# Optimization experiments

Hardware: AMD Instinct MI355X
Metric: run time of the kernel (lower is better)

Reference implementation:

```python
import jax, jax.numpy as jnp
import numpy as np

B, T, N, C = 32, 16, 1000, 16   # batch, seq_len, num_nodes, in_channels
G, H, O = 32, 512, 8            # gcn_hidden, lstm_hidden, output_dim
E_RAND = 8000                   # random edges; + N self loops -> E = 9000


def setup_inputs() -> dict:
    key = jax.random.key(0)
    ks = jax.random.split(key, 13)
    rng = np.random.default_rng(0)
    src = rng.integers(0, N, E_RAND)
    dst = rng.integers(0, N, E_RAND)
    loop = np.arange(N)
    edge_index = jnp.asarray(
        np.stack([np.concatenate([src, loop]), np.concatenate([dst, loop])]),
        dtype=jnp.int32)
    ew = np.concatenate([rng.uniform(0.5, 1.5, E_RAND), np.ones(N)]).astype(np.float32)

    def p(k, s, sc):
        return jax.random.normal(k, s, jnp.float32) * sc

    return {
        'x': p(ks[0], (B, T, N, C), 1.0),
        'edge_index': edge_index,
        'edge_weight': jnp.asarray(ew),
        'gcn_w': p(ks[1], (T, C, G), 0.1),
        'gcn_b': p(ks[2], (T, G), 0.02),
        'w_ih0': p(ks[3], (4 * H, N * G), 0.02),
        'w_hh0': p(ks[4], (4 * H, H), 0.02),
        'b_ih0': p(ks[5], (4 * H,), 0.02),
        'b_hh0': p(ks[6], (4 * H,), 0.02),
        'w_ih1': p(ks[7], (4 * H, H), 0.02),
        'w_hh1': p(ks[8], (4 * H, H), 0.02),
        'b_ih1': p(ks[9], (4 * H,), 0.02),
        'b_hh1': p(ks[10], (4 * H,), 0.02),
        'proj_w': p(ks[11], (O, H), 0.04),
        'proj_b': p(ks[12], (O,), 0.02),
    }


def _lstm_layer(inp, w_ih, w_hh, b_ih, b_hh):
    # inp: [B, T, D]; torch gate order i, f, g, o
    pre = jnp.einsum('btd,gd->btg', inp, w_ih) + b_ih + b_hh  # [B, T, 4H]
    h0 = jnp.zeros((inp.shape[0], w_hh.shape[1]), inp.dtype)

    def step(carry, x_t):
        h, c = carry
        gates = x_t + h @ w_hh.T
        i, f, g, o = jnp.split(gates, 4, axis=-1)
        c = jax.nn.sigmoid(f) * c + jax.nn.sigmoid(i) * jnp.tanh(g)
        h = jax.nn.sigmoid(o) * jnp.tanh(c)
        return (h, c), h

    _, hs = jax.lax.scan(step, (h0, h0), pre.transpose(1, 0, 2))  # [T, B, H]
    return hs.transpose(1, 0, 2)


def reference(x, edge_index, edge_weight, gcn_w, gcn_b,
              w_ih0, w_hh0, b_ih0, b_hh0,
              w_ih1, w_hh1, b_ih1, b_hh1, proj_w, proj_b):
    src, dst = edge_index[0], edge_index[1]
    # GCN symmetric normalization (self-loops already present in edge list)
    deg = jax.ops.segment_sum(edge_weight, dst, num_segments=N)
    dinv = jnp.where(deg > 0, jax.lax.rsqrt(jnp.maximum(deg, 1e-12)), 0.0)
    norm = dinv[src] * edge_weight * dinv[dst]  # [E]
    # per-timestep linear transform: distinct GCN weight per t
    xw = jnp.einsum('btni,tio->btno', x, gcn_w)  # [B, T, N, G]
    # gather from source nodes, scale, scatter-add into targets
    msg = xw[:, :, src, :] * norm[None, None, :, None]      # [B, T, E, G]
    agg = jnp.zeros_like(xw).at[:, :, dst, :].add(msg)      # [B, T, N, G]
    h = jax.nn.relu(agg + gcn_b[None, :, None, :])
    seq = h.reshape(B, T, N * G)                            # [B, T, N*G]
    out1 = _lstm_layer(seq, w_ih0, w_hh0, b_ih0, b_hh0)
    out2 = _lstm_layer(out1, w_ih1, w_hh1, b_ih1, b_hh1)
    last = out2[:, -1, :]                                   # [B, H]
    return last @ proj_w.T + proj_b                         # [B, O]
```

## Files before the change

### kernel.cpp

```cpp
#include <hip/hip_runtime.h>
#include <hip/hip_bf16.h>

typedef unsigned short u16;
typedef __bf16 bf16x8 __attribute__((ext_vector_type(8)));
typedef float f32x4 __attribute__((ext_vector_type(4)));
typedef unsigned short u16x8 __attribute__((ext_vector_type(8)));
typedef unsigned long long u64;

#define NB 32
#define NT 16
#define NN 1000
#define NC 16
#define NG 32
#define NH 512
#define NK 32000
#define BH (NB*NH)
#define LWG 64
#define LTH 384
#define NSPLIT 8

__device__ __forceinline__ u16 f2bf(float f) {
    unsigned int u = __float_as_uint(f);
    unsigned int r = u + 0x7FFFu + ((u >> 16) & 1u);
    return (u16)(r >> 16);
}

__device__ __forceinline__ unsigned cvt2(float a, float b) {
    unsigned r;
    asm("v_cvt_pk_bf16_f32 %0, %1, %2" : "=v"(r) : "v"(a), "v"(b));
    return r;
}

__device__ __forceinline__ float sigmoidf(float x) { return 1.f / (1.f + __expf(-x)); }

__device__ __forceinline__ float dot4(float4 a, float4 b) {
    return a.x * b.x + a.y * b.y + a.z * b.z + a.w * b.w;
}

#define AT_LOAD(p)    __hip_atomic_load((p), __ATOMIC_RELAXED, __HIP_MEMORY_SCOPE_AGENT)
#define AT_STORE(p,v) __hip_atomic_store((p), (v), __ATOMIC_RELAXED, __HIP_MEMORY_SCOPE_AGENT)

#define GLOAD16(g, l) __builtin_amdgcn_global_load_lds( \
    (const __attribute__((address_space(1))) void*)(g),  \
    (__attribute__((address_space(3))) void*)(l), 16, 0, 0)

__global__ void graph_prep(const int* __restrict__ ei, const float* __restrict__ ew, int E,
                           int* __restrict__ rowptr, int* __restrict__ csr_src,
                           float* __restrict__ csr_nrm) {
    __shared__ float degs[NN];
    __shared__ float dinv[NN];
    __shared__ int cnt[NN];
    __shared__ int rp[NN + 1];
    __shared__ int wsum[16];
    int tid = threadIdx.x, lane = tid & 63, wid = tid >> 6;
    for (int n = tid; n < NN; n += 1024) { degs[n] = 0.f; cnt[n] = 0; }
    __syncthreads();
    for (int e = tid; e < E; e += 1024) {
        int d = ei[E + e];
        atomicAdd(&degs[d], ew[e]);
        atomicAdd(&cnt[d], 1);
    }
    __syncthreads();
    for (int n = tid; n < NN; n += 1024) {
        float d = degs[n];
        dinv[n] = d > 0.f ? rsqrtf(fmaxf(d, 1e-12f)) : 0.f;
    }
    int v = (tid < NN) ? cnt[tid] : 0;
    int inc = v;
#pragma unroll
    for (int d = 1; d < 64; d <<= 1) {
        int u = __shfl_up(inc, d, 64);
        if (lane >= d) inc += u;
    }
    if (lane == 63) wsum[wid] = inc;
    __syncthreads();
    if (tid == 0) {
        int a = 0;
#pragma unroll
        for (int i = 0; i < 16; ++i) { int t = wsum[i]; wsum[i] = a; a += t; }
    }
    __syncthreads();
    int excl = inc - v + wsum[wid];
    if (tid <= NN) { rp[tid] = excl; rowptr[tid] = excl; }
    if (tid < NN) cnt[tid] = 0;
    __syncthreads();
    for (int e = tid; e < E; e += 1024) {
        int d = ei[E + e], s = ei[e];
        int pos = rp[d] + atomicAdd(&cnt[d], 1);
        csr_src[pos] = s;
        csr_nrm[pos] = dinv[s] * ew[e] * dinv[d];
    }
}

__global__ __launch_bounds__(1024) void gcn_fused(const float* __restrict__ x,
                                                  const float* __restrict__ gw,
                                                  const float* __restrict__ gb,
                                                  const int* __restrict__ rowptr,
                                                  const int* __restrict__ csr_src,
                                                  const float* __restrict__ csr_nrm,
                                                  u16* __restrict__ seq) {
    __shared__ float xwlds[NN * NG];
    __shared__ float wlds[NC * NG];
    __shared__ int rplds[NN + 1];
    int bt = blockIdx.x;
    int t = bt & 15;
    int tid = threadIdx.x;
    int g = tid & 31, grp = tid >> 5;

    for (int i = tid; i < NC * NG; i += 1024) wlds[i] = gw[t * NC * NG + i];
    for (int i = tid; i <= NN; i += 1024) rplds[i] = rowptr[i];
    __syncthreads();

    const float* xbt = x + (size_t)bt * NN * NC;
    for (int r = grp; r < NN; r += 32) {
        const float4* xr = (const float4*)(xbt + r * NC);
        float4 a0 = xr[0], a1 = xr[1], a2 = xr[2], a3 = xr[3];
        float acc = a0.x * wlds[g]        + a0.y * wlds[32 + g]
                  + a0.z * wlds[64 + g]   + a0.w * wlds[96 + g]
                  + a1.x * wlds[128 + g]  + a1.y * wlds[160 + g]
                  + a1.z * wlds[192 + g]  + a1.w * wlds[224 + g]
                  + a2.x * wlds[256 + g]  + a2.y * wlds[288 + g]
                  + a2.z * wlds[320 + g]  + a2.w * wlds[352 + g]
                  + a3.x * wlds[384 + g]  + a3.y * wlds[416 + g]
                  + a3.z * wlds[448 + g]  + a3.w * wlds[480 + g];
        xwlds[r * NG + g] = acc;
    }
    __syncthreads();

    float bias = gb[t * NG + g];
    u16* seqbt = seq + (size_t)bt * NK;
    for (int n = grp; n < NN; n += 32) {
        int p0 = rplds[n], p1 = rplds[n + 1];
        float acc = 0.f;
        for (int p = p0; p < p1; ++p)
            acc += csr_nrm[p] * xwlds[csr_src[p] * NG + g];
        seqbt[n * NG + g] = f2bf(fmaxf(acc + bias, 0.f));
    }
}

__global__ __launch_bounds__(256) void gemm_f32b(const u16* __restrict__ A,
                                                 const float* __restrict__ Bw,
                                                 float* __restrict__ part) {
    __shared__ __align__(16) u16 As[2][128 * 64];
    __shared__ __align__(16) u16 Bs[2][128 * 64];
    int tid = threadIdx.x;
    int lane = tid & 63, wid = tid >> 6;
    int wr = wid >> 1, wc = wid & 1;
    int bid = blockIdx.x;
    int s = bid & 7;
    int idx = bid >> 3;
    int tm = (idx & 3) * 128, tn = (idx >> 2) * 128;
    int ks0 = s * 62 + (s < 4 ? s : 4);
    int ksn = (s < 4) ? 63 : 62;

    int srow = tid >> 3, sc = tid & 7;
    int sce = sc ^ (srow & 7);
    const u16* gaBase = A + (size_t)(tm + srow) * NK + (size_t)ks0 * 64 + sce * 8;
    int br = tid >> 3, bc = tid & 7;
    int bce = bc ^ (br & 7);
    const float* gbBase = Bw + (size_t)(tn + br) * NK + (size_t)ks0 * 64 + bce * 8;

    f32x4 acc[4][4];
#pragma unroll
    for (int i = 0; i < 4; ++i)
#pragma unroll
        for (int j = 0; j < 4; ++j) acc[i][j] = (f32x4){0.f, 0.f, 0.f, 0.f};

    int fr = lane & 15, kq = lane >> 4, fs = fr & 7;

    float4 bq0[4], bq1[4];
#pragma unroll
    for (int q = 0; q < 4; ++q)
        GLOAD16(gaBase + (size_t)q * 32 * NK, &As[0][0] + srow * 64 + sc * 8 + q * 32 * 64);
#pragma unroll
    for (int q = 0; q < 4; ++q) {
        bq0[q] = *(const float4*)(gbBase + (size_t)q * 32 * NK);
        bq1[q] = *(const float4*)(gbBase + (size_t)q * 32 * NK + 4);
    }
#pragma unroll
    for (int q = 0; q < 4; ++q) {
        uint4 w;
        w.x = cvt2(bq0[q].x, bq0[q].y); w.y = cvt2(bq0[q].z, bq0[q].w);
        w.z = cvt2(bq1[q].x, bq1[q].y); w.w = cvt2(bq1[q].z, bq1[q].w);
        *(uint4*)(&Bs[0][0] + (br + q * 32) * 64 + bc * 8) = w;
    }
    __syncthreads();

    int p = 0;
    for (int ks = 0; ks < ksn; ++ks) {
        bool more = (ks + 1) < ksn;
        if (more) {
            const u16* ga = gaBase + (size_t)(ks + 1) * 64;
#pragma unroll
            for (int q = 0; q < 4; ++q)
                GLOAD16(ga + (size_t)q * 32 * NK, &As[p ^ 1][0] + srow * 64 + sc * 8 + q * 32 * 64);
            const float* gbf = gbBase + (size_t)(ks + 1) * 64;
#pragma unroll
            for (int q = 0; q < 4; ++q) {
                bq0[q] = *(const float4*)(gbf + (size_t)q * 32 * NK);
                bq1[q] = *(const float4*)(gbf + (size_t)q * 32 * NK + 4);
            }
        }
        {
            const u16* Ap = &As[p][0];
            const u16* Bp = &Bs[p][0];
#pragma unroll
            for (int kk = 0; kk < 2; ++kk) {
                int c0 = ((kq + kk * 4) ^ fs) * 8;
                bf16x8 af[4], bv[4];
#pragma unroll
                for (int fm = 0; fm < 4; ++fm)
                    af[fm] = *(const bf16x8*)(Ap + (wr * 64 + fm * 16 + fr) * 64 + c0);
#pragma unroll
                for (int fn = 0; fn < 4; ++fn)
                    bv[fn] = *(const bf16x8*)(Bp + (wc * 64 + fn * 16 + fr) * 64 + c0);
#pragma unroll
                for (int fm = 0; fm < 4; ++fm)
#pragma unroll
                    for (int fn = 0; fn < 4; ++fn)
                        acc[fm][fn] = __builtin_amdgcn_mfma_f32_16x16x32_bf16(af[fm], bv[fn], acc[fm][fn], 0, 0, 0);
            }
        }
        if (more) {
#pragma unroll
            for (int q = 0; q < 4; ++q) {
                uint4 w;
                w.x = cvt2(bq0[q].x, bq0[q].y); w.y = cvt2(bq0[q].z, bq0[q].w);
                w.z = cvt2(bq1[q].x, bq1[q].y); w.w = cvt2(bq1[q].z, bq1[q].w);
                *(uint4*)(&Bs[p ^ 1][0] + (br + q * 32) * 64 + bc * 8) = w;
            }
        }
        __syncthreads();
        p ^= 1;
    }

    int rq = lane >> 4;
    size_t base = (size_t)s * 512 * 2048;
#pragma unroll
    for (int fm = 0; fm < 4; ++fm)
#pragma unroll
        for (int fn = 0; fn < 4; ++fn)
#pragma unroll
            for (int rr = 0; rr < 4; ++rr) {
                int m = tm + wr * 64 + fm * 16 + rq * 4 + rr;
                int n = tn + wc * 64 + fn * 16 + (lane & 15);
                part[base + (size_t)m * 2048 + n] = acc[fm][fn][rr];
            }
}

__global__ __launch_bounds__(256) void reduce_bias_p(const float* __restrict__ part,
                                                     const float* __restrict__ b_ih0,
                                                     const float* __restrict__ b_hh0,
                                                     float* __restrict__ pre0p) {
    int s = blockIdx.y;
    int r = blockIdx.x * 64 + (threadIdx.x & 63);
    int bq = threadIdx.x >> 6;
    float bias = b_ih0[r] + b_hh0[r];
#pragma unroll
    for (int b8 = 0; b8 < 8; ++b8) {
        int b = bq * 8 + b8;
        float acc = bias;
#pragma unroll
        for (int sk = 0; sk < NSPLIT; ++sk)
            acc += part[(size_t)sk * 1048576 + (size_t)(b * 16 + s) * 2048 + r];
        pre0p[((size_t)s * 2048 + r) * 32 + b] = acc;
    }
}

__global__ __launch_bounds__(256) void wperm(const float* __restrict__ w_hh0,
                                             const float* __restrict__ w_ih1,
                                             const float* __restrict__ w_hh1,
                                             u16* __restrict__ Wbig) {
    int rt = blockIdx.x;
    int wg = blockIdx.y;
    int tid = threadIdx.x;
#pragma unroll
    for (int it = 0; it < 4; ++it) {
        int idx = it * 256 + tid;
        int kt = idx >> 6, lane = idx & 63;
        int p = rt * 16 + (lane & 15);
        int gate = (p & 31) >> 3;
        int col = wg * 8 + (p & 7);
        const float* src;
        if (p < 32)      src = w_hh0 + (size_t)(gate * NH + col) * NH;
        else if (p < 64) src = w_ih1 + (size_t)(gate * NH + col) * NH;
        else             src = w_hh1 + (size_t)(gate * NH + col) * NH;
        int k0 = kt * 32 + (lane >> 4) * 8;
        float4 v0 = *(const float4*)(src + k0);
        float4 v1 = *(const float4*)(src + k0 + 4);
        u16x8 o;
        o[0] = f2bf(v0.x); o[1] = f2bf(v0.y); o[2] = f2bf(v0.z); o[3] = f2bf(v0.w);
        o[4] = f2bf(v1.x); o[5] = f2bf(v1.y); o[6] = f2bf(v1.z); o[7] = f2bf(v1.w);
        *(u16x8*)(Wbig + (((size_t)wg * 6 + rt) * 16 + kt) * 512 + lane * 8) = o;
    }
}

__global__ void init2(u16* h0, u16* h1, int* flags) {
    int i = blockIdx.x * 256 + threadIdx.x;
    if (i < 2 * BH) { h0[i] = 0; h1[i] = 0; }
    if (i < 1024) flags[i] = 0;
}

__global__ __launch_bounds__(LTH) void lstm2(const u16* __restrict__ Wbig,
                                             const float* __restrict__ pre0p,
                                             const float* __restrict__ b_ih1,
                                             const float* __restrict__ b_hh1,
                                             u16* __restrict__ h0buf,
                                             u16* __restrict__ h1buf,
                                             float* __restrict__ h1f,
                                             int* __restrict__ flags) {
    __shared__ __align__(16) u16 hA0[32 * 520];
    __shared__ __align__(16) u16 hA1[32 * 520];
    __shared__ float G[96][33];
    __shared__ float cst[2][8][32];
    __shared__ u16 hst[2][8][32];
    int wg = blockIdx.x, tid = threadIdx.x;
    int wid = tid >> 6, lane = tid & 63;
    int grp = wid >> 1;

    bf16x8 af[16];
    const u16* wsrc = Wbig + (size_t)wg * 49152 + wid * 8192 + lane * 8;
#pragma unroll
    for (int kt = 0; kt < 16; ++kt) af[kt] = *(const bf16x8*)(wsrc + kt * 512);

    if (tid < 512) ((float*)cst)[tid] = 0.f;

    int uj = (tid >> 5) & 7, ub = tid & 31;
    int ucol = wg * 8 + uj;
    float bs0 = 0.f, bs1 = 0.f, bs2 = 0.f, bs3 = 0.f;
    if (tid < 256) {
        bs0 = b_ih1[ucol] + b_hh1[ucol];
        bs1 = b_ih1[NH + ucol] + b_hh1[NH + ucol];
        bs2 = b_ih1[2 * NH + ucol] + b_hh1[2 * NH + ucol];
        bs3 = b_ih1[3 * NH + ucol] + b_hh1[3 * NH + ucol];
    }
    __syncthreads();

    for (int s = 0; s <= 16; ++s) {
        for (int r = wid; r < 64; r += 6) {
            const u64* src = (r < 32)
                ? (const u64*)(h0buf + ((s & 1) ^ 1) * BH + r * 512)
                : (const u64*)(h1buf + (s & 1) * BH + (r - 32) * 512);
            u16* dst = (r < 32) ? (hA0 + r * 520) : (hA1 + (r - 32) * 520);
            u64 v0 = AT_LOAD(src + lane);
            u64 v1 = AT_LOAD(src + 64 + lane);
            *(u64*)(dst + lane * 4) = v0;
            *(u64*)(dst + 256 + lane * 4) = v1;
        }
        float up0 = 0.f, up1 = 0.f, up2 = 0.f, up3 = 0.f;
        if (tid < 256 && s < 16) {
            const float* pp = pre0p + (size_t)s * 2048 * 32 + ub;
            up0 = pp[(size_t)ucol * 32];
            up1 = pp[((size_t)NH + ucol) * 32];
            up2 = pp[((size_t)2 * NH + ucol) * 32];
            up3 = pp[((size_t)3 * NH + ucol) * 32];
        }
        __syncthreads();

        bool active = (grp == 0) ? (s < 16) : (s >= 1);
        if (active) {
            const u16* hA = (grp < 2) ? hA0 : hA1;
            const u16* hp = hA + (lane & 15) * 520 + (lane >> 4) * 8;
            f32x4 a0 = (f32x4){0.f, 0.f, 0.f, 0.f};
            f32x4 a1 = (f32x4){0.f, 0.f, 0.f, 0.f};
#pragma unroll
            for (int kt = 0; kt < 16; ++kt) {
                bf16x8 b0 = *(const bf16x8*)(hp + kt * 32);
                bf16x8 b1 = *(const bf16x8*)(hp + 16 * 520 + kt * 32);
                a0 = __builtin_amdgcn_mfma_f32_16x16x32_bf16(af[kt], b0, a0, 0, 0, 0);
                a1 = __builtin_amdgcn_mfma_f32_16x16x32_bf16(af[kt], b1, a1, 0, 0, 0);
            }
            int r0 = wid * 16 + (lane >> 4) * 4;
#pragma unroll
            for (int rr = 0; rr < 4; ++rr) {
                G[r0 + rr][lane & 15] = a0[rr];
                G[r0 + rr][16 + (lane & 15)] = a1[rr];
            }
        }
        __syncthreads();

        if (tid < 256) {
            if (s < 16) {
                float gi = G[uj][ub] + up0;
                float gf = G[8 + uj][ub] + up1;
                float gg = G[16 + uj][ub] + up2;
                float go = G[24 + uj][ub] + up3;
                float c = sigmoidf(gf) * cst[0][uj][ub] + sigmoidf(gi) * tanhf(gg);
                cst[0][uj][ub] = c;
                hst[0][uj][ub] = f2bf(sigmoidf(go) * tanhf(c));
            }
            if (s >= 1) {
                float gi = G[32 + uj][ub] + G[64 + uj][ub] + bs0;
                float gf = G[40 + uj][ub] + G[72 + uj][ub] + bs1;
                float gg = G[48 + uj][ub] + G[80 + uj][ub] + bs2;
                float go = G[56 + uj][ub] + G[88 + uj][ub] + bs3;
                float c = sigmoidf(gf) * cst[1][uj][ub] + sigmoidf(gi) * tanhf(gg);
                cst[1][uj][ub] = c;
                float hv = sigmoidf(go) * tanhf(c);
                hst[1][uj][ub] = f2bf(hv);
                if (s == 16) h1f[ub * NH + ucol] = hv;
            }
        }
        __syncthreads();

        if (s < 16) {
            if (wid == 0) {
                if (lane < 32) {
                    union { u16 a[8]; u64 q[2]; } v;
#pragma unroll
                    for (int j = 0; j < 8; ++j) v.a[j] = hst[0][j][lane];
                    u64* d = (u64*)(h0buf + (s & 1) * BH + lane * 512 + wg * 8);
                    AT_STORE(d, v.q[0]); AT_STORE(d + 1, v.q[1]);
                } else if (s >= 1) {
                    int b = lane - 32;
                    union { u16 a[8]; u64 q[2]; } v;
#pragma unroll
                    for (int j = 0; j < 8; ++j) v.a[j] = hst[1][j][b];
                    u64* d = (u64*)(h1buf + ((s - 1) & 1) * BH + b * 512 + wg * 8);
                    AT_STORE(d, v.q[0]); AT_STORE(d + 1, v.q[1]);
                }
                asm volatile("s_waitcnt vmcnt(0)" ::: "memory");
                if (lane == 0) AT_STORE(&flags[wg * 16], s + 1);
                int target = s + 1;
                for (;;) {
                    int v = AT_LOAD(&flags[lane * 16]);
                    if (__all(v >= target)) break;
                    __builtin_amdgcn_s_sleep(1);
                }
            }
            __syncthreads();
        }
    }
}

__global__ __launch_bounds__(1024) void proj_k(const float* __restrict__ h1f,
                                               const float* __restrict__ proj_w,
                                               const float* __restrict__ proj_b,
                                               float* __restrict__ out) {
    __shared__ float pj[32][8][4];
    int tid = threadIdx.x;
    int b = tid >> 5, o = (tid >> 2) & 7, kq = tid & 3;
    const float4* hp = (const float4*)(h1f + (size_t)b * NH + kq * 128);
    const float4* wp = (const float4*)(proj_w + (size_t)o * NH + kq * 128);
    float acc = 0.f;
#pragma unroll 8
    for (int k = 0; k < 32; ++k) acc += dot4(hp[k], wp[k]);
    pj[b][o][kq] = acc;
    __syncthreads();
    if (tid < 256) {
        int bb = tid >> 3, oo = tid & 7;
        out[bb * 8 + oo] = pj[bb][oo][0] + pj[bb][oo][1] + pj[bb][oo][2] + pj[bb][oo][3] + proj_b[oo];
    }
}

extern "C" void kernel_launch(void* const* d_in, const int* in_sizes, int n_in,
                              void* d_out, int out_size, void* d_ws, size_t ws_size,
                              hipStream_t stream) {
    const float* x      = (const float*)d_in[0];
    const int*   ei     = (const int*)d_in[1];
    const float* ew     = (const float*)d_in[2];
    const float* gcn_w  = (const float*)d_in[3];
    const float* gcn_b  = (const float*)d_in[4];
    const float* w_ih0  = (const float*)d_in[5];
    const float* w_hh0  = (const float*)d_in[6];
    const float* b_ih0  = (const float*)d_in[7];
    const float* b_hh0  = (const float*)d_in[8];
    const float* w_ih1  = (const float*)d_in[9];
    const float* w_hh1  = (const float*)d_in[10];
    const float* b_ih1  = (const float*)d_in[11];
    const float* b_hh1  = (const float*)d_in[12];
    const float* proj_w = (const float*)d_in[13];
    const float* proj_b = (const float*)d_in[14];
    int E = in_sizes[2];

    char* ws = (char*)d_ws;
    size_t off = 0;
    float* part   = (float*)(ws + off);
    u16* Wbig     = (u16*)part;        off += 50331648;
    u16* seq      = (u16*)(ws + off);  off += 32768000;
    float* pre0p  = (float*)(ws + off); off += 4194304;
    u16* h0buf    = (u16*)(ws + off);  off += 2 * BH * 2;
    u16* h1buf    = (u16*)(ws + off);  off += 2 * BH * 2;
    float* h1f    = (float*)(ws + off); off += BH * 4;
    int* flags    = (int*)(ws + off);  off += 4096;
    int* rowptr   = (int*)(ws + off);  off += 4096;
    int* csr_src  = (int*)(ws + off);  off += 36864;
    float* csr_nrm = (float*)(ws + off); off += 36864;
    (void)ws_size; (void)n_in; (void)out_size;

    graph_prep<<<1, 1024, 0, stream>>>(ei, ew, E, rowptr, csr_src, csr_nrm);
    gcn_fused<<<512, 1024, 0, stream>>>(x, gcn_w, gcn_b, rowptr, csr_src, csr_nrm, seq);
    gemm_f32b<<<512, 256, 0, stream>>>(seq, w_ih0, part);
    reduce_bias_p<<<dim3(32, 16), 256, 0, stream>>>(part, b_ih0, b_hh0, pre0p);
    wperm<<<dim3(6, 64), 256, 0, stream>>>(w_hh0, w_ih1, w_hh1, Wbig);
    init2<<<128, 256, 0, stream>>>(h0buf, h1buf, flags);

    lstm2<<<LWG, LTH, 0, stream>>>(Wbig, pre0p, b_ih1, b_hh1, h0buf, h1buf, h1f, flags);
    proj_k<<<1, 1024, 0, stream>>>(h1f, proj_w, proj_b, (float*)d_out);
}
```

Baseline: 462.7 us.

## Deepen split-K GEMM pipeline: prefetch fp32 B two tiles ahead with manual waitcnt

Restructures the split-K GEMM mainloop so the fp32 weight tile loads are issued two k-steps ahead into alternating register sets, while the bf16 A tile is still async-loaded one step ahead into LDS. The __syncthreads is replaced with an explicit s_waitcnt vmcnt(8)/lgkmcnt(0) plus s_barrier, so the newest B loads can stay in flight across the barrier. The loop is unrolled by two to ping-pong the register buffers, and tail steps reload clamped tiles instead of branching. The aim is to hide global load latency of the large weight stream. The cost is extra register pressure and redundant loads at the tail, and the hand-counted vmcnt could be wrong if the compiler reorders memory ops.

```diff
diff --git a/kernel.cpp b/kernel.cpp
--- a/kernel.cpp
+++ b/kernel.cpp
@@ -168,71 +168,83 @@
 
     int fr = lane & 15, kq = lane >> 4, fs = fr & 7;
 
-    float4 bq0[4], bq1[4];
-#pragma unroll
-    for (int q = 0; q < 4; ++q)
-        GLOAD16(gaBase + (size_t)q * 32 * NK, &As[0][0] + srow * 64 + sc * 8 + q * 32 * 64);
-#pragma unroll
-    for (int q = 0; q < 4; ++q) {
-        bq0[q] = *(const float4*)(gbBase + (size_t)q * 32 * NK);
-        bq1[q] = *(const float4*)(gbBase + (size_t)q * 32 * NK + 4);
-    }
-#pragma unroll
-    for (int q = 0; q < 4; ++q) {
-        uint4 w;
-        w.x = cvt2(bq0[q].x, bq0[q].y); w.y = cvt2(bq0[q].z, bq0[q].w);
-        w.z = cvt2(bq1[q].x, bq1[q].y); w.w = cvt2(bq1[q].z, bq1[q].w);
-        *(uint4*)(&Bs[0][0] + (br + q * 32) * 64 + bc * 8) = w;
-    }
-    __syncthreads();
-
-    int p = 0;
-    for (int ks = 0; ks < ksn; ++ks) {
-        bool more = (ks + 1) < ksn;
-        if (more) {
-            const u16* ga = gaBase + (size_t)(ks + 1) * 64;
-#pragma unroll
-            for (int q = 0; q < 4; ++q)
-                GLOAD16(ga + (size_t)q * 32 * NK, &As[p ^ 1][0] + srow * 64 + sc * 8 + q * 32 * 64);
-            const float* gbf = gbBase + (size_t)(ks + 1) * 64;
-#pragma unroll
-            for (int q = 0; q < 4; ++q) {
-                bq0[q] = *(const float4*)(gbf + (size_t)q * 32 * NK);
-                bq1[q] = *(const float4*)(gbf + (size_t)q * 32 * NK + 4);
-            }
-        }
-        {
-            const u16* Ap = &As[p][0];
-            const u16* Bp = &Bs[p][0];
-#pragma unroll
-            for (int kk = 0; kk < 2; ++kk) {
-                int c0 = ((kq + kk * 4) ^ fs) * 8;
-                bf16x8 af[4], bv[4];
-#pragma unroll
-                for (int fm = 0; fm < 4; ++fm)
-                    af[fm] = *(const bf16x8*)(Ap + (wr * 64 + fm * 16 + fr) * 64 + c0);
+    float4 bqA[8], bqB[8];
+
+    auto issueA = [&](int kt, int buf) {
+#pragma unroll
+        for (int q = 0; q < 4; ++q)
+            GLOAD16(gaBase + (size_t)kt * 64 + (size_t)q * 32 * NK,
+                    &As[buf][0] + srow * 64 + sc * 8 + q * 32 * 64);
+    };
+    auto loadB = [&](int kt, float4* dst) {
+        const float* g = gbBase + (size_t)kt * 64;
+#pragma unroll
+        for (int q = 0; q < 4; ++q) {
+            dst[2 * q]     = *(const float4*)(g + (size_t)q * 32 * NK);
+            dst[2 * q + 1] = *(const float4*)(g + (size_t)q * 32 * NK + 4);
+        }
+    };
+    auto cvtB = [&](const float4* src, int buf) {
+#pragma unroll
+        for (int q = 0; q < 4; ++q) {
+            uint4 w;
+            w.x = cvt2(src[2 * q].x, src[2 * q].y);
+            w.y = cvt2(src[2 * q].z, src[2 * q].w);
+            w.z = cvt2(src[2 * q + 1].x, src[2 * q + 1].y);
+            w.w = cvt2(src[2 * q + 1].z, src[2 * q + 1].w);
+            *(uint4*)(&Bs[buf][0] + (br + q * 32) * 64 + bc * 8) = w;
+        }
+    };
+    auto mfmaStep = [&](int buf) {
+        const u16* Ap = &As[buf][0];
+        const u16* Bp = &Bs[buf][0];
+#pragma unroll
+        for (int kk = 0; kk < 2; ++kk) {
+            int c0 = ((kq + kk * 4) ^ fs) * 8;
+            bf16x8 af[4], bv[4];
+#pragma unroll
+            for (int fm = 0; fm < 4; ++fm)
+                af[fm] = *(const bf16x8*)(Ap + (wr * 64 + fm * 16 + fr) * 64 + c0);
+#pragma unroll
+            for (int fn = 0; fn < 4; ++fn)
+                bv[fn] = *(const bf16x8*)(Bp + (wc * 64 + fn * 16 + fr) * 64 + c0);
+#pragma unroll
+            for (int fm = 0; fm < 4; ++fm)
 #pragma unroll
                 for (int fn = 0; fn < 4; ++fn)
-                    bv[fn] = *(const bf16x8*)(Bp + (wc * 64 + fn * 16 + fr) * 64 + c0);
-#pragma unroll
-                for (int fm = 0; fm < 4; ++fm)
-#pragma unroll
-                    for (int fn = 0; fn < 4; ++fn)
-                        acc[fm][fn] = __builtin_amdgcn_mfma_f32_16x16x32_bf16(af[fm], bv[fn], acc[fm][fn], 0, 0, 0);
-            }
-        }
-        if (more) {
-#pragma unroll
-            for (int q = 0; q < 4; ++q) {
-                uint4 w;
-                w.x = cvt2(bq0[q].x, bq0[q].y); w.y = cvt2(bq0[q].z, bq0[q].w);
-                w.z = cvt2(bq1[q].x, bq1[q].y); w.w = cvt2(bq1[q].z, bq1[q].w);
-                *(uint4*)(&Bs[p ^ 1][0] + (br + q * 32) * 64 + bc * 8) = w;
-            }
-        }
-        __syncthreads();
-        p ^= 1;
-    }
+                    acc[fm][fn] = __builtin_amdgcn_mfma_f32_16x16x32_bf16(af[fm], bv[fn], acc[fm][fn], 0, 0, 0);
+        }
+    };
+
+    issueA(0, 0);
+    loadB(0, bqA);
+    loadB(ksn > 1 ? 1 : 0, bqB);
+    cvtB(bqA, 0);
+    asm volatile("s_waitcnt lgkmcnt(0)" ::: "memory");
+    asm volatile("s_barrier" ::: "memory");
+
+#define STEP(KS, P, CUR, NXT)                                                  \
+    {                                                                          \
+        int kA = (KS) + 1 < ksn ? (KS) + 1 : ksn - 1;                          \
+        int kB = (KS) + 2 < ksn ? (KS) + 2 : ksn - 1;                          \
+        issueA(kA, (P) ^ 1);                         \
+        loadB(kB, NXT);                     \
+        mfmaStep(P);                                                           \
+        cvtB(CUR, (P) ^ 1);                    \
+        asm volatile("s_waitcnt vmcnt(8) lgkmcnt(0)" ::: "memory");            \
+        asm volatile("s_barrier" ::: "memory");                                \
+    }
+
+    int ks = 0;
+    while (ks + 2 <= ksn) {
+        STEP(ks, 0, bqB, bqA);
+        STEP(ks + 1, 1, bqA, bqB);
+        ks += 2;
+    }
+    if (ks < ksn) {
+        STEP(ks, 0, bqB, bqA);
+    }
+#undef STEP
 
     int rq = lane >> 4;
     size_t base = (size_t)s * 512 * 2048;
```

Result: faster. 444.0 us (-4.0%).
